# Optimization experiments

Measured on AMD Instinct MI355X. Metric: run time of the kernel, lower is better.

The kernel has to match this reference:

```python
import jax, jax.numpy as jnp
import numpy as np

NEG_SLOPE = 0.01  # F.leaky_relu default
EPS = 1e-12       # F.normalize default eps


def neigh_agg(x, edges, num_node, W, b):
    # x: [N, D]; edges: [2, E] (src, tgt); returns [num_node, D]
    src, tgt = edges[0], edges[1]
    h = jax.nn.relu(x @ W + b)                 # [N, D]
    msgs = h[tgt]                              # [E, D] gather
    aggr = jax.ops.segment_sum(msgs, src, num_segments=num_node)  # scatter-add
    deg = jax.ops.segment_sum(jnp.ones(src.shape, h.dtype), src, num_segments=num_node)
    deg = jnp.clip(deg, 1.0)                   # clamp(min=1)
    return aggr / deg[:, None]                 # dropout omitted (eval mode)


def setup_inputs() -> dict:
    key = jax.random.key(0)
    ks = jax.random.split(key, 20)
    N, D, E = 50000, 128, 1600000
    inp = {}
    for i, r in enumerate("gdcs"):
        inp[f"x_{r}"] = jax.random.normal(ks[i], (N, D), jnp.float32)
        inp[f"edges_{r}"] = jax.random.randint(ks[4 + i], (2, E), 0, N, jnp.int32)
    inp["x_node"] = jax.random.normal(ks[8], (N, D), jnp.float32)
    inp["num_node"] = N
    s = 1.0 / np.sqrt(D)
    for i, r in enumerate("gdcs"):
        inp[f"W_{r}"] = jax.random.uniform(ks[9 + 2 * i], (D, D), jnp.float32, -s, s)
        inp[f"b_{r}"] = jax.random.uniform(ks[10 + 2 * i], (D,), jnp.float32, -s, s)
    inp["u"] = jax.random.normal(ks[17], (2 * D, 1), jnp.float32)
    s2 = 1.0 / np.sqrt(2 * D)
    inp["W_lin"] = jax.random.uniform(ks[18], (2 * D, D), jnp.float32, -s2, s2)
    inp["b_lin"] = jax.random.uniform(ks[19], (D,), jnp.float32, -s2, s2)
    return inp


def reference(x_g, x_d, x_c, x_s, edges_g, edges_d, edges_c, edges_s, x_node,
              num_node, W_g, b_g, W_d, b_d, W_c, b_c, W_s, b_s, u, W_lin, b_lin):
    aggrs = [
        neigh_agg(x_g, edges_g, num_node, W_g, b_g),
        neigh_agg(x_d, edges_d, num_node, W_d, b_d),
        neigh_agg(x_c, edges_c, num_node, W_c, b_c),
        neigh_agg(x_s, edges_s, num_node, W_s, b_s),
    ]
    # attention scores per relation: exp(leaky_relu([aggr, x_node] @ u))
    scores = [jnp.exp(jax.nn.leaky_relu(jnp.concatenate([a, x_node], axis=-1) @ u,
                                        NEG_SLOPE)) for a in aggrs]  # each [N,1]
    denom = scores[0] + scores[1] + scores[2] + scores[3]
    combined = sum((s / denom) * a for s, a in zip(scores, aggrs))   # [N, D]
    y = jax.nn.relu(jnp.concatenate([x_node, combined], axis=-1) @ W_lin + b_lin)
    norm = jnp.maximum(jnp.linalg.norm(y, axis=-1, keepdims=True), EPS)
    return y / norm
```

## Files before the change

### kernel.cpp

```cpp
#include <hip/hip_runtime.h>
#include <hip/hip_fp16.h>
#include <cstddef>


#define BN1       512
#define BN1_SHIFT 9
#define BCAP1     20480
#define NB1MAX    128
#define BLK_E     8192

struct IP4 { const int* p[4]; };
struct FP4 { const float* p[4]; };

typedef _Float16 half8 __attribute__((ext_vector_type(8)));
typedef float f32x4 __attribute__((ext_vector_type(4)));
typedef float f32x2 __attribute__((ext_vector_type(2)));

__global__ __launch_bounds__(256) void prep0_k(FP4 Wm, const float* __restrict__ Wl,
                                               __half* __restrict__ Wt,
                                               __half* __restrict__ Wlt,
                                               int* __restrict__ bcur, int nzero) {
    const int b = blockIdx.x, t = threadIdx.x;
    if (b < 256) {
        int r = b >> 6;
        int i = (b & 63) * 256 + t;
        int k = i & 127, c = i >> 7;
        Wt[(size_t)r * 16384 + c * 128 + k] = __float2half(Wm.p[r][(size_t)k * 128 + c]);
    } else if (b < 384) {
        int i = (b - 256) * 256 + t;
        int k = i & 255, c = i >> 8;
        Wlt[(size_t)c * 256 + k] = __float2half(Wl[(size_t)k * 128 + c]);
    } else {
        for (int i = (b - 384) * 256 + t; i < nzero; i += 64 * 256) bcur[i] = 0;
    }
}

__global__ __launch_bounds__(256) void binGemm_k(IP4 ed, int4 Ev, int* __restrict__ bcur,
                                                 int* __restrict__ staging, int nb1, int binb,
                                                 FP4 X, const __half* __restrict__ Wt,
                                                 FP4 Bv, unsigned char* __restrict__ H8,
                                                 int M, int gb) {
    __shared__ int ldsu[4096];
    const int t = threadIdx.x;
    const int x = blockIdx.x;

    if (x < 4 * binb) {
        const int r = x / binb;
        const int bx = x - r * binb;
        const int E = (r == 0) ? Ev.x : (r == 1) ? Ev.y : (r == 2) ? Ev.z : Ev.w;
        const int e0 = bx * BLK_E;
        if (e0 >= E) return;
        const int e1 = min(e0 + BLK_E, E);
        const int* es = ed.p[r];
        const int* et = es + E;
        int* bc = bcur + (size_t)r * nb1 * 16;
        int* stg = staging + (size_t)r * nb1 * BCAP1;
        int* hist = ldsu;
        int* curs = ldsu + NB1MAX;

        for (int b = t; b < nb1; b += 256) hist[b] = 0;
        __syncthreads();
        {
            const int n = e1 - e0;
            const int n4 = n >> 2;
            const int4* s4 = reinterpret_cast<const int4*>(es + e0);
            for (int i = t; i < n4; i += 256) {
                int4 s = s4[i];
                atomicAdd(&hist[s.x >> BN1_SHIFT], 1);
                atomicAdd(&hist[s.y >> BN1_SHIFT], 1);
                atomicAdd(&hist[s.z >> BN1_SHIFT], 1);
                atomicAdd(&hist[s.w >> BN1_SHIFT], 1);
            }
            for (int i = e0 + n4 * 4 + t; i < e1; i += 256)
                atomicAdd(&hist[es[i] >> BN1_SHIFT], 1);
        }
        __syncthreads();
        for (int b = t; b < nb1; b += 256) {
            int c = hist[b];
            curs[b] = c ? atomicAdd(&bc[b * 16], c) : 0;
        }
        __syncthreads();
        {
            const int n = e1 - e0;
            const int n4 = n >> 2;
            const int4* s4 = reinterpret_cast<const int4*>(es + e0);
            const int4* t4 = reinterpret_cast<const int4*>(et + e0);
            for (int i = t; i < n4; i += 256) {
                int4 s = s4[i];
                int4 tg = t4[i];
                int b, p;
                b = s.x >> BN1_SHIFT; p = atomicAdd(&curs[b], 1);
                if (p < BCAP1) stg[(size_t)b * BCAP1 + p] = ((s.x & 511) << 16) | tg.x;
                b = s.y >> BN1_SHIFT; p = atomicAdd(&curs[b], 1);
                if (p < BCAP1) stg[(size_t)b * BCAP1 + p] = ((s.y & 511) << 16) | tg.y;
                b = s.z >> BN1_SHIFT; p = atomicAdd(&curs[b], 1);
                if (p < BCAP1) stg[(size_t)b * BCAP1 + p] = ((s.z & 511) << 16) | tg.z;
                b = s.w >> BN1_SHIFT; p = atomicAdd(&curs[b], 1);
                if (p < BCAP1) stg[(size_t)b * BCAP1 + p] = ((s.w & 511) << 16) | tg.w;
            }
            for (int i = e0 + n4 * 4 + t; i < e1; i += 256) {
                int s = es[i];
                int b = s >> BN1_SHIFT;
                int p = atomicAdd(&curs[b], 1);
                if (p < BCAP1) stg[(size_t)b * BCAP1 + p] = ((s & 511) << 16) | et[i];
            }
        }
    } else {
        const int g = x - 4 * binb;
        const int r = g / gb;
        const int bx = g - r * gb;
        const float* A = X.p[r];
        const __half* Wr = Wt + (size_t)r * 16384;
        const float* bias = Bv.p[r];
        unsigned char* Hr = H8 + (size_t)r * M * 128;
        const int n0 = bx * 64;
        char* AsB = reinterpret_cast<char*>(ldsu);

        for (int s = t; s < 1024; s += 256) {
            int row = s >> 4, c8 = (s & 15) << 3;
            int grow = n0 + row;
            float4 v0 = make_float4(0.f, 0.f, 0.f, 0.f), v1 = v0;
            if (grow < M) {
                v0 = *reinterpret_cast<const float4*>(&A[(size_t)grow * 128 + c8]);
                v1 = *reinterpret_cast<const float4*>(&A[(size_t)grow * 128 + c8 + 4]);
            }
            half8 hv;
            hv[0] = (_Float16)v0.x; hv[1] = (_Float16)v0.y;
            hv[2] = (_Float16)v0.z; hv[3] = (_Float16)v0.w;
            hv[4] = (_Float16)v1.x; hv[5] = (_Float16)v1.y;
            hv[6] = (_Float16)v1.z; hv[7] = (_Float16)v1.w;
            int byte = (row * 256 + c8 * 2) ^ ((row & 7) << 4);
            *reinterpret_cast<half8*>(AsB + byte) = hv;
        }
        __syncthreads();

        const int w = t >> 6, lane = t & 63;
        const int r0 = (w & 1) * 32, c0 = (w >> 1) * 64;
        const int lr = lane & 15;
        const int lk = (lane >> 4) * 8;

        f32x4 acc[2][4] = {};
        #pragma unroll
        for (int k0 = 0; k0 < 128; k0 += 32) {
            half8 af[2], bf[4];
            #pragma unroll
            for (int mi = 0; mi < 2; ++mi) {
                int row = r0 + mi * 16 + lr;
                int byte = (row * 256 + (k0 + lk) * 2) ^ ((row & 7) << 4);
                af[mi] = *reinterpret_cast<const half8*>(AsB + byte);
            }
            #pragma unroll
            for (int ni = 0; ni < 4; ++ni) {
                int col = c0 + ni * 16 + lr;
                bf[ni] = *reinterpret_cast<const half8*>(&Wr[(size_t)col * 128 + k0 + lk]);
            }
            #pragma unroll
            for (int mi = 0; mi < 2; ++mi)
                #pragma unroll
                for (int ni = 0; ni < 4; ++ni)
                    acc[mi][ni] = __builtin_amdgcn_mfma_f32_16x16x32_f16(af[mi], bf[ni],
                                                                         acc[mi][ni], 0, 0, 0);
        }
        __syncthreads();
        unsigned char* ht = reinterpret_cast<unsigned char*>(AsB);
        #pragma unroll
        for (int ni = 0; ni < 4; ++ni) {
            int col = c0 + ni * 16 + lr;
            float bb = bias[col];
            #pragma unroll
            for (int mi = 0; mi < 2; ++mi) {
                #pragma unroll
                for (int j = 0; j < 4; ++j) {
                    int row = r0 + mi * 16 + (lane >> 4) * 4 + j;
                    float y = fmaxf(acc[mi][ni][j] + bb, 0.f);
                    int e = __builtin_amdgcn_cvt_pk_fp8_f32(y, 0.f, 0, false);
                    ht[row * 128 + col] = (unsigned char)e;
                }
            }
        }
        __syncthreads();
        {
            int row = t >> 2, cb = (t & 3) * 32;
            int grow = n0 + row;
            if (grow < M) {
                const int4* p = reinterpret_cast<const int4*>(ht + row * 128 + cb);
                int4 a = p[0], b = p[1];
                int4* q = reinterpret_cast<int4*>(Hr + (size_t)grow * 128 + cb);
                q[0] = a; q[1] = b;
            }
        }
    }
}

__global__ __launch_bounds__(1024) void bscan_k(const int* __restrict__ bcur,
                                                int* __restrict__ bbase, int total) {
    __shared__ int wsum[16];
    __shared__ int carry_s;
    if (threadIdx.x == 0) carry_s = 0;
    __syncthreads();
    const int lane = threadIdx.x & 63, wid = threadIdx.x >> 6;
    for (int base = 0; base < total; base += 1024) {
        int i = base + threadIdx.x;
        int v = (i < total) ? min(bcur[(size_t)i * 16], BCAP1) : 0;
        int incl = v;
        #pragma unroll
        for (int d = 1; d < 64; d <<= 1) {
            int t = __shfl_up(incl, d);
            if (lane >= d) incl += t;
        }
        if (lane == 63) wsum[wid] = incl;
        __syncthreads();
        if (wid == 0 && lane < 16) {
            int w = wsum[lane];
            int wi = w;
            #pragma unroll
            for (int d = 1; d < 16; d <<= 1) {
                int t = __shfl_up(wi, d);
                if (lane >= d) wi += t;
            }
            wsum[lane] = wi - w;
        }
        __syncthreads();
        int excl = carry_s + wsum[wid] + incl - v;
        if (i < total) bbase[(size_t)i * 16] = excl;
        __syncthreads();
        if (threadIdx.x == 1023) carry_s = excl + v;
        __syncthreads();
    }
}

__global__ __launch_bounds__(256) void csr2_k(const int* __restrict__ staging,
                                              const int* __restrict__ bcur,
                                              const int* __restrict__ bbase,
                                              int* __restrict__ counts,
                                              int* __restrict__ offsets,
                                              int* __restrict__ sorted,
                                              int nb1, int N) {
    const int r = blockIdx.y;
    const int b = blockIdx.x;
    const int gi = r * nb1 + b;
    const int sz = min(bcur[(size_t)gi * 16], BCAP1);
    const int base = bbase[(size_t)gi * 16];
    const int* stg = staging + (size_t)gi * BCAP1;
    const int nbase = b * BN1;
    const int t = threadIdx.x;
    const int lane = t & 63, wid = t >> 6;

    __shared__ int hist[BN1];
    __shared__ int cur[BN1];
    __shared__ int wsum[4];

    hist[t] = 0;
    hist[t + 256] = 0;
    __syncthreads();
    {
        const int sz4 = sz >> 2;
        const int4* s4 = reinterpret_cast<const int4*>(stg);
        for (int i = t; i < sz4; i += 256) {
            int4 v = s4[i];
            atomicAdd(&hist[((unsigned)v.x) >> 16], 1);
            atomicAdd(&hist[((unsigned)v.y) >> 16], 1);
            atomicAdd(&hist[((unsigned)v.z) >> 16], 1);
            atomicAdd(&hist[((unsigned)v.w) >> 16], 1);
        }
        for (int i = sz4 * 4 + t; i < sz; i += 256)
            atomicAdd(&hist[((unsigned)stg[i]) >> 16], 1);
    }
    __syncthreads();
    int v0 = hist[2 * t], v1 = hist[2 * t + 1];
    int ps = v0 + v1;
    int incl = ps;
    #pragma unroll
    for (int d = 1; d < 64; d <<= 1) {
        int x = __shfl_up(incl, d);
        if (lane >= d) incl += x;
    }
    if (lane == 63) wsum[wid] = incl;
    __syncthreads();
    if (t == 0) {
        int a = 0;
        #pragma unroll
        for (int i = 0; i < 4; ++i) { int x = wsum[i]; wsum[i] = a; a += x; }
    }
    __syncthreads();
    int e0 = wsum[wid] + incl - ps;
    cur[2 * t] = e0;
    cur[2 * t + 1] = e0 + v0;
    {
        int n0 = nbase + 2 * t;
        if (n0 < N) {
            counts[(size_t)r * N + n0] = v0;
            offsets[(size_t)r * N + n0] = base + e0;
        }
        if (n0 + 1 < N) {
            counts[(size_t)r * N + n0 + 1] = v1;
            offsets[(size_t)r * N + n0 + 1] = base + e0 + v0;
        }
    }
    __syncthreads();
    for (int i = t; i < sz; i += 256) {
        int rec = stg[i];
        int p = atomicAdd(&cur[((unsigned)rec) >> 16], 1);
        sorted[base + p] = rec & 0xFFFF;
    }
}

__global__ __launch_bounds__(256) void gather_attn_k(const unsigned char* __restrict__ H8,
                                                     const float* __restrict__ xn,
                                                     const float* __restrict__ u,
                                                     const int* __restrict__ offsets,
                                                     const int* __restrict__ counts,
                                                     const int* __restrict__ sorted,
                                                     __half* __restrict__ comb, int N) {
    const int node = blockIdx.x * 4 + (threadIdx.x >> 6);
    if (node >= N) return;
    const int lane = threadIdx.x & 63;
    const int q = lane >> 4;
    const int c = lane & 15;

    float2 x2 = *reinterpret_cast<const float2*>(&xn[(size_t)node * 128 + lane * 2]);
    float2 ux = *reinterpret_cast<const float2*>(&u[128 + lane * 2]);
    float px = x2.x * ux.x + x2.y * ux.y;
    #pragma unroll
    for (int m = 1; m < 64; m <<= 1) px += __shfl_xor(px, m);

    float4 ua0 = reinterpret_cast<const float4*>(u)[c * 2];
    float4 ua1 = reinterpret_cast<const float4*>(u)[c * 2 + 1];

    float a[4][8];
    float invd[4], pr[4];
    #pragma unroll
    for (int r = 0; r < 4; ++r) {
        const int beg = offsets[(size_t)r * N + node];
        const int cnt = counts[(size_t)r * N + node];
        const unsigned char* hr = H8 + (size_t)r * N * 128;
        const int* sl = sorted + beg;
        f32x2 s01 = {0.f, 0.f}, s23 = {0.f, 0.f}, s45 = {0.f, 0.f}, s67 = {0.f, 0.f};
        int my = (lane < cnt) ? sl[lane] : 0;
        for (int j0 = 0; j0 < cnt; j0 += 64) {
            const int m = min(64, cnt - j0);
            int my_next = (j0 + 64 + lane < cnt) ? sl[j0 + 64 + lane] : 0;
            int j = 0;
            for (; j + 8 <= m; j += 8) {
                int tg0 = __shfl(my, j + q);
                int tg1 = __shfl(my, j + q + 4);
                uint2 raw0 = reinterpret_cast<const uint2*>(hr + (size_t)tg0 * 128)[c];
                uint2 raw1 = reinterpret_cast<const uint2*>(hr + (size_t)tg1 * 128)[c];
                s01 += __builtin_amdgcn_cvt_pk_f32_fp8((int)raw0.x, false);
                s23 += __builtin_amdgcn_cvt_pk_f32_fp8((int)raw0.x, true);
                s45 += __builtin_amdgcn_cvt_pk_f32_fp8((int)raw0.y, false);
                s67 += __builtin_amdgcn_cvt_pk_f32_fp8((int)raw0.y, true);
                s01 += __builtin_amdgcn_cvt_pk_f32_fp8((int)raw1.x, false);
                s23 += __builtin_amdgcn_cvt_pk_f32_fp8((int)raw1.x, true);
                s45 += __builtin_amdgcn_cvt_pk_f32_fp8((int)raw1.y, false);
                s67 += __builtin_amdgcn_cvt_pk_f32_fp8((int)raw1.y, true);
            }
            for (; j < m; j += 4) {
                int jj = j + q;
                int tg = __shfl(my, min(jj, m - 1));
                if (jj < m) {
                    uint2 raw = reinterpret_cast<const uint2*>(hr + (size_t)tg * 128)[c];
                    s01 += __builtin_amdgcn_cvt_pk_f32_fp8((int)raw.x, false);
                    s23 += __builtin_amdgcn_cvt_pk_f32_fp8((int)raw.x, true);
                    s45 += __builtin_amdgcn_cvt_pk_f32_fp8((int)raw.y, false);
                    s67 += __builtin_amdgcn_cvt_pk_f32_fp8((int)raw.y, true);
                }
            }
            my = my_next;
        }
        float s[8] = {s01[0], s01[1], s23[0], s23[1], s45[0], s45[1], s67[0], s67[1]};
        #pragma unroll
        for (int k = 0; k < 8; ++k) {
            s[k] += __shfl_xor(s[k], 16);
            s[k] += __shfl_xor(s[k], 32);
        }
        float dp = s[0] * ua0.x + s[1] * ua0.y + s[2] * ua0.z + s[3] * ua0.w
                 + s[4] * ua1.x + s[5] * ua1.y + s[6] * ua1.z + s[7] * ua1.w;
        #pragma unroll
        for (int m = 1; m < 16; m <<= 1) dp += __shfl_xor(dp, m);
        pr[r] = dp;
        invd[r] = 1.0f / fmaxf((float)cnt, 1.0f);
        #pragma unroll
        for (int k = 0; k < 8; ++k) a[r][k] = s[k];
    }
    float wgt[4], denom = 0.f;
    #pragma unroll
    for (int r = 0; r < 4; ++r) {
        float sc = pr[r] * invd[r] + px;
        float z = (sc > 0.f) ? sc : 0.01f * sc;
        wgt[r] = expf(z);
        denom += wgt[r];
    }
    float cf[4];
    #pragma unroll
    for (int r = 0; r < 4; ++r) cf[r] = (wgt[r] / denom) * invd[r];
    if (q == 0) {
        half8 o;
        #pragma unroll
        for (int k = 0; k < 8; ++k)
            o[k] = (_Float16)(cf[0] * a[0][k] + cf[1] * a[1][k] +
                              cf[2] * a[2][k] + cf[3] * a[3][k]);
        *reinterpret_cast<half8*>(&comb[(size_t)node * 128 + c * 8]) = o;
    }
}

__global__ __launch_bounds__(256) void gemm_out_k(const float* __restrict__ Xn,
                                                  const __half* __restrict__ Cb,
                                                  const __half* __restrict__ Wlt,
                                                  const float* __restrict__ bias,
                                                  float* __restrict__ out, int M) {
    __shared__ __half As[64 * 128];
    __shared__ float rowss[64];
    const int t = threadIdx.x;
    const int n0 = blockIdx.x * 64;
    char* AsB = reinterpret_cast<char*>(As);
    if (t < 64) rowss[t] = 0.f;

    const int w = t >> 6, lane = t & 63;
    const int r0 = (w & 1) * 32, c0 = (w >> 1) * 64;
    const int lr = lane & 15;
    const int lk = (lane >> 4) * 8;

    f32x4 acc[2][4] = {};
    #pragma unroll
    for (int p = 0; p < 2; ++p) {
        if (p == 0) {
            for (int s = t; s < 1024; s += 256) {
                int row = s >> 4, c8 = (s & 15) << 3;
                int grow = n0 + row;
                float4 v0 = make_float4(0.f, 0.f, 0.f, 0.f), v1 = v0;
                if (grow < M) {
                    v0 = *reinterpret_cast<const float4*>(&Xn[(size_t)grow * 128 + c8]);
                    v1 = *reinterpret_cast<const float4*>(&Xn[(size_t)grow * 128 + c8 + 4]);
                }
                half8 hv;
                hv[0] = (_Float16)v0.x; hv[1] = (_Float16)v0.y;
                hv[2] = (_Float16)v0.z; hv[3] = (_Float16)v0.w;
                hv[4] = (_Float16)v1.x; hv[5] = (_Float16)v1.y;
                hv[6] = (_Float16)v1.z; hv[7] = (_Float16)v1.w;
                int byte = (row * 256 + c8 * 2) ^ ((row & 7) << 4);
                *reinterpret_cast<half8*>(AsB + byte) = hv;
            }
        } else {
            for (int s = t; s < 1024; s += 256) {
                int row = s >> 4, c8 = (s & 15) << 3;
                int grow = n0 + row;
                half8 hv = {};
                if (grow < M) hv = *reinterpret_cast<const half8*>(&Cb[(size_t)grow * 128 + c8]);
                int byte = (row * 256 + c8 * 2) ^ ((row & 7) << 4);
                *reinterpret_cast<half8*>(AsB + byte) = hv;
            }
        }
        __syncthreads();
        #pragma unroll
        for (int k0 = 0; k0 < 128; k0 += 32) {
            half8 af[2], bf[4];
            #pragma unroll
            for (int mi = 0; mi < 2; ++mi) {
                int row = r0 + mi * 16 + lr;
                int byte = (row * 256 + (k0 + lk) * 2) ^ ((row & 7) << 4);
                af[mi] = *reinterpret_cast<const half8*>(AsB + byte);
            }
            #pragma unroll
            for (int ni = 0; ni < 4; ++ni) {
                int col = c0 + ni * 16 + lr;
                bf[ni] = *reinterpret_cast<const half8*>(&Wlt[(size_t)col * 256 + p * 128 + k0 + lk]);
            }
            #pragma unroll
            for (int mi = 0; mi < 2; ++mi)
                #pragma unroll
                for (int ni = 0; ni < 4; ++ni)
                    acc[mi][ni] = __builtin_amdgcn_mfma_f32_16x16x32_f16(af[mi], bf[ni],
                                                                         acc[mi][ni], 0, 0, 0);
        }
        __syncthreads();
    }
    float bbv[4];
    #pragma unroll
    for (int ni = 0; ni < 4; ++ni) bbv[ni] = bias[c0 + ni * 16 + lr];
    #pragma unroll
    for (int mi = 0; mi < 2; ++mi) {
        #pragma unroll
        for (int j = 0; j < 4; ++j) {
            int row_l = r0 + mi * 16 + (lane >> 4) * 4 + j;
            float ss = 0.f;
            #pragma unroll
            for (int ni = 0; ni < 4; ++ni) {
                float y = fmaxf(acc[mi][ni][j] + bbv[ni], 0.f);
                ss += y * y;
            }
            ss += __shfl_xor(ss, 1); ss += __shfl_xor(ss, 2);
            ss += __shfl_xor(ss, 4); ss += __shfl_xor(ss, 8);
            if (lr == 0) atomicAdd(&rowss[row_l], ss);
        }
    }
    __syncthreads();
    #pragma unroll
    for (int mi = 0; mi < 2; ++mi) {
        #pragma unroll
        for (int j = 0; j < 4; ++j) {
            int row_l = r0 + mi * 16 + (lane >> 4) * 4 + j;
            int grow = n0 + row_l;
            if (grow < M) {
                float inv = 1.0f / fmaxf(sqrtf(rowss[row_l]), 1e-12f);
                #pragma unroll
                for (int ni = 0; ni < 4; ++ni) {
                    float y = fmaxf(acc[mi][ni][j] + bbv[ni], 0.f);
                    out[(size_t)grow * 128 + c0 + ni * 16 + lr] = y * inv;
                }
            }
        }
    }
}

extern "C" void kernel_launch(void* const* d_in, const int* in_sizes, int n_in,
                              void* d_out, int out_size, void* d_ws, size_t ws_size,
                              hipStream_t stream) {
    FP4 X  = {{(const float*)d_in[0], (const float*)d_in[2],
               (const float*)d_in[4], (const float*)d_in[6]}};
    IP4 ED = {{(const int*)d_in[1], (const int*)d_in[3],
               (const int*)d_in[5], (const int*)d_in[7]}};
    const float* xn = (const float*)d_in[8];
    FP4 Wm = {{(const float*)d_in[10], (const float*)d_in[12],
               (const float*)d_in[14], (const float*)d_in[16]}};
    FP4 Bv = {{(const float*)d_in[11], (const float*)d_in[13],
               (const float*)d_in[15], (const float*)d_in[17]}};
    const float* u  = (const float*)d_in[18];
    const float* Wl = (const float*)d_in[19];
    const float* bl = (const float*)d_in[20];
    float* out = (float*)d_out;

    const int N = in_sizes[8] / 128;
    int E[4];
    for (int r = 0; r < 4; ++r) E[r] = in_sizes[1 + 2 * r] / 2;
    const int4 Ev = make_int4(E[0], E[1], E[2], E[3]);
    const int nb1 = (N + BN1 - 1) / BN1;
    int maxE = 0;
    for (int r = 0; r < 4; ++r) maxE = (E[r] > maxE) ? E[r] : maxE;

    unsigned char* h8 = (unsigned char*)d_ws;
    char*  ubase   = (char*)(h8 + (size_t)4 * N * 128);
    int*   staging = (int*)ubase;
    __half* comb   = (__half*)ubase;
    size_t usz = (size_t)4 * nb1 * BCAP1 * sizeof(int);
    size_t csz = (size_t)N * 128 * sizeof(__half);
    char*  after   = ubase + (usz > csz ? usz : csz);
    __half* Wt     = (__half*)after;
    __half* Wlt    = Wt + (size_t)4 * 16384;
    int* offsets = (int*)(Wlt + (size_t)128 * 256);
    int* counts  = offsets + (size_t)4 * N;
    int* bcur    = counts + (size_t)4 * N;
    int* bbase   = bcur + (size_t)4 * nb1 * 16;
    int* sorted  = bbase + (size_t)4 * nb1 * 16;

    const int gb = (N + 63) / 64;
    const int binb = (maxE + BLK_E - 1) / BLK_E;

    prep0_k<<<448, 256, 0, stream>>>(Wm, Wl, Wt, Wlt, bcur, 4 * nb1 * 16);
    binGemm_k<<<4 * binb + 4 * gb, 256, 0, stream>>>(ED, Ev, bcur, staging, nb1, binb,
                                                     X, Wt, Bv, h8, N, gb);
    bscan_k<<<1, 1024, 0, stream>>>(bcur, bbase, 4 * nb1);
    csr2_k<<<dim3(nb1, 4), 256, 0, stream>>>(staging, bcur, bbase, counts, offsets,
                                             sorted, nb1, N);
    gather_attn_k<<<(N + 3) / 4, 256, 0, stream>>>(h8, xn, u, offsets, counts, sorted,
                                                   comb, N);
    gemm_out_k<<<gb, 256, 0, stream>>>(xn, comb, Wlt, bl, out, N);
}
```

Measured before the change: 324.4 us.

## Replace bucket scan kernel with atomic base allocation and compact CSR arrays

Measured after the change: 303.5 us. 1.07x faster.

```diff
diff --git a/kernel.cpp b/kernel.cpp
--- a/kernel.cpp
+++ b/kernel.cpp
@@ -7,7 +7,7 @@
 #define BN1_SHIFT 9
 #define BCAP1     20480
 #define NB1MAX    128
-#define BLK_E     8192
+#define BLK_E     16384
 
 struct IP4 { const int* p[4]; };
 struct FP4 { const float* p[4]; };
@@ -192,55 +192,16 @@
     }
 }
 
-__global__ __launch_bounds__(1024) void bscan_k(const int* __restrict__ bcur,
-                                                int* __restrict__ bbase, int total) {
-    __shared__ int wsum[16];
-    __shared__ int carry_s;
-    if (threadIdx.x == 0) carry_s = 0;
-    __syncthreads();
-    const int lane = threadIdx.x & 63, wid = threadIdx.x >> 6;
-    for (int base = 0; base < total; base += 1024) {
-        int i = base + threadIdx.x;
-        int v = (i < total) ? min(bcur[(size_t)i * 16], BCAP1) : 0;
-        int incl = v;
-        #pragma unroll
-        for (int d = 1; d < 64; d <<= 1) {
-            int t = __shfl_up(incl, d);
-            if (lane >= d) incl += t;
-        }
-        if (lane == 63) wsum[wid] = incl;
-        __syncthreads();
-        if (wid == 0 && lane < 16) {
-            int w = wsum[lane];
-            int wi = w;
-            #pragma unroll
-            for (int d = 1; d < 16; d <<= 1) {
-                int t = __shfl_up(wi, d);
-                if (lane >= d) wi += t;
-            }
-            wsum[lane] = wi - w;
-        }
-        __syncthreads();
-        int excl = carry_s + wsum[wid] + incl - v;
-        if (i < total) bbase[(size_t)i * 16] = excl;
-        __syncthreads();
-        if (threadIdx.x == 1023) carry_s = excl + v;
-        __syncthreads();
-    }
-}
-
 __global__ __launch_bounds__(256) void csr2_k(const int* __restrict__ staging,
                                               const int* __restrict__ bcur,
-                                              const int* __restrict__ bbase,
-                                              int* __restrict__ counts,
-                                              int* __restrict__ offsets,
-                                              int* __restrict__ sorted,
+                                              int* __restrict__ gcur,
+                                              int2* __restrict__ offc,
+                                              unsigned short* __restrict__ sorted,
                                               int nb1, int N) {
     const int r = blockIdx.y;
     const int b = blockIdx.x;
     const int gi = r * nb1 + b;
     const int sz = min(bcur[(size_t)gi * 16], BCAP1);
-    const int base = bbase[(size_t)gi * 16];
     const int* stg = staging + (size_t)gi * BCAP1;
     const int nbase = b * BN1;
     const int t = threadIdx.x;
@@ -249,7 +210,9 @@
     __shared__ int hist[BN1];
     __shared__ int cur[BN1];
     __shared__ int wsum[4];
-
+    __shared__ int base_s;
+
+    if (t == 0) base_s = atomicAdd(gcur, sz);
     hist[t] = 0;
     hist[t + 256] = 0;
     __syncthreads();
@@ -267,6 +230,7 @@
             atomicAdd(&hist[((unsigned)stg[i]) >> 16], 1);
     }
     __syncthreads();
+    const int base = base_s;
     int v0 = hist[2 * t], v1 = hist[2 * t + 1];
     int ps = v0 + v1;
     int incl = ps;
@@ -288,29 +252,38 @@
     cur[2 * t + 1] = e0 + v0;
     {
         int n0 = nbase + 2 * t;
-        if (n0 < N) {
-            counts[(size_t)r * N + n0] = v0;
-            offsets[(size_t)r * N + n0] = base + e0;
-        }
-        if (n0 + 1 < N) {
-            counts[(size_t)r * N + n0 + 1] = v1;
-            offsets[(size_t)r * N + n0 + 1] = base + e0 + v0;
-        }
+        if (n0 < N) offc[(size_t)r * N + n0] = make_int2(base + e0, v0);
+        if (n0 + 1 < N) offc[(size_t)r * N + n0 + 1] = make_int2(base + e0 + v0, v1);
     }
     __syncthreads();
-    for (int i = t; i < sz; i += 256) {
-        int rec = stg[i];
-        int p = atomicAdd(&cur[((unsigned)rec) >> 16], 1);
-        sorted[base + p] = rec & 0xFFFF;
+    {
+        const int sz4 = sz >> 2;
+        const int4* s4 = reinterpret_cast<const int4*>(stg);
+        for (int i = t; i < sz4; i += 256) {
+            int4 v = s4[i];
+            int p;
+            p = atomicAdd(&cur[((unsigned)v.x) >> 16], 1);
+            sorted[base + p] = (unsigned short)(v.x & 0xFFFF);
+            p = atomicAdd(&cur[((unsigned)v.y) >> 16], 1);
+            sorted[base + p] = (unsigned short)(v.y & 0xFFFF);
+            p = atomicAdd(&cur[((unsigned)v.z) >> 16], 1);
+            sorted[base + p] = (unsigned short)(v.z & 0xFFFF);
+            p = atomicAdd(&cur[((unsigned)v.w) >> 16], 1);
+            sorted[base + p] = (unsigned short)(v.w & 0xFFFF);
+        }
+        for (int i = sz4 * 4 + t; i < sz; i += 256) {
+            int rec = stg[i];
+            int p = atomicAdd(&cur[((unsigned)rec) >> 16], 1);
+            sorted[base + p] = (unsigned short)(rec & 0xFFFF);
+        }
     }
 }
 
 __global__ __launch_bounds__(256) void gather_attn_k(const unsigned char* __restrict__ H8,
                                                      const float* __restrict__ xn,
                                                      const float* __restrict__ u,
-                                                     const int* __restrict__ offsets,
-                                                     const int* __restrict__ counts,
-                                                     const int* __restrict__ sorted,
+                                                     const int2* __restrict__ offc,
+                                                     const unsigned short* __restrict__ sorted,
                                                      __half* __restrict__ comb, int N) {
     const int node = blockIdx.x * 4 + (threadIdx.x >> 6);
     if (node >= N) return;
@@ -331,15 +304,15 @@
     float invd[4], pr[4];
     #pragma unroll
     for (int r = 0; r < 4; ++r) {
-        const int beg = offsets[(size_t)r * N + node];
-        const int cnt = counts[(size_t)r * N + node];
+        const int2 oc = offc[(size_t)r * N + node];
+        const int beg = oc.x, cnt = oc.y;
         const unsigned char* hr = H8 + (size_t)r * N * 128;
-        const int* sl = sorted + beg;
+        const unsigned short* sl = sorted + beg;
         f32x2 s01 = {0.f, 0.f}, s23 = {0.f, 0.f}, s45 = {0.f, 0.f}, s67 = {0.f, 0.f};
-        int my = (lane < cnt) ? sl[lane] : 0;
+        int my = (lane < cnt) ? (int)sl[lane] : 0;
         for (int j0 = 0; j0 < cnt; j0 += 64) {
             const int m = min(64, cnt - j0);
-            int my_next = (j0 + 64 + lane < cnt) ? sl[j0 + 64 + lane] : 0;
+            int my_next = (j0 + 64 + lane < cnt) ? (int)sl[j0 + 64 + lane] : 0;
             int j = 0;
             for (; j + 8 <= m; j += 8) {
                 int tg0 = __shfl(my, j + q);
@@ -547,22 +520,18 @@
     char*  after   = ubase + (usz > csz ? usz : csz);
     __half* Wt     = (__half*)after;
     __half* Wlt    = Wt + (size_t)4 * 16384;
-    int* offsets = (int*)(Wlt + (size_t)128 * 256);
-    int* counts  = offsets + (size_t)4 * N;
-    int* bcur    = counts + (size_t)4 * N;
-    int* bbase   = bcur + (size_t)4 * nb1 * 16;
-    int* sorted  = bbase + (size_t)4 * nb1 * 16;
+    int2* offc   = (int2*)(Wlt + (size_t)128 * 256);
+    int* bcur    = (int*)(offc + (size_t)4 * N);
+    int* gcur    = bcur + (size_t)4 * nb1 * 16;
+    unsigned short* sorted = (unsigned short*)(gcur + 16);
 
     const int gb = (N + 63) / 64;
     const int binb = (maxE + BLK_E - 1) / BLK_E;
 
-    prep0_k<<<448, 256, 0, stream>>>(Wm, Wl, Wt, Wlt, bcur, 4 * nb1 * 16);
+    prep0_k<<<448, 256, 0, stream>>>(Wm, Wl, Wt, Wlt, bcur, 4 * nb1 * 16 + 16);
     binGemm_k<<<4 * binb + 4 * gb, 256, 0, stream>>>(ED, Ev, bcur, staging, nb1, binb,
                                                      X, Wt, Bv, h8, N, gb);
-    bscan_k<<<1, 1024, 0, stream>>>(bcur, bbase, 4 * nb1);
-    csr2_k<<<dim3(nb1, 4), 256, 0, stream>>>(staging, bcur, bbase, counts, offsets,
-                                             sorted, nb1, N);
-    gather_attn_k<<<(N + 3) / 4, 256, 0, stream>>>(h8, xn, u, offsets, counts, sorted,
-                                                   comb, N);
+    csr2_k<<<dim3(nb1, 4), 256, 0, stream>>>(staging, bcur, gcur, offc, sorted, nb1, N);
+    gather_attn_k<<<(N + 3) / 4, 256, 0, stream>>>(h8, xn, u, offc, sorted, comb, N);
     gemm_out_k<<<gb, 256, 0, stream>>>(xn, comb, Wlt, bl, out, N);
 }
```
